# Optimization experiments

Measured on AMD Instinct MI355X. Metric: run time of the kernel, lower is better.

The kernel has to match this reference:

```python
import jax, jax.numpy as jnp
import numpy as np

N = 100000   # nodes
E = 1600000  # edges
IN = 128     # input feature dim
HID = 64     # hidden = IN // 2
OUT = 8      # output_size
B = 16384    # lookup batch


def sage_conv(x, src, dst, W_l, W_r, b, n):
    # PyG SAGEConv (aggr='mean', root_weight=True):
    # out = lin_l(mean_{j in N(i)} x_j) + lin_r(x_i)
    msgs = x[src]                                              # [E, F] gather
    agg = jax.ops.segment_sum(msgs, dst, num_segments=n)       # [N, F] scatter-add
    deg = jax.ops.segment_sum(jnp.ones((src.shape[0],), x.dtype), dst, num_segments=n)
    mean = agg / jnp.maximum(deg, 1.0)[:, None]                # zero-degree -> 0
    return mean @ W_l + x @ W_r + b


def setup_inputs() -> dict:
    key = jax.random.key(0)
    ks = jax.random.split(key, 10)
    node_feats = jax.random.normal(ks[0], (N, IN), dtype=jnp.float32)
    edge_index = jax.random.randint(ks[1], (2, E), 0, N, dtype=jnp.int64)
    idx = jax.random.randint(ks[2], (B,), 0, N, dtype=jnp.int64)
    dropout_mask = jax.random.uniform(ks[3], (N, HID), dtype=jnp.float32)
    s1 = 1.0 / np.sqrt(IN)
    s2 = 1.0 / np.sqrt(HID)
    W1_l = jax.random.normal(ks[4], (IN, HID), dtype=jnp.float32) * s1
    W1_r = jax.random.normal(ks[5], (IN, HID), dtype=jnp.float32) * s1
    b1 = jnp.zeros((HID,), dtype=jnp.float32)
    W2_l = jax.random.normal(ks[6], (HID, OUT), dtype=jnp.float32) * s2
    W2_r = jax.random.normal(ks[7], (HID, OUT), dtype=jnp.float32) * s2
    b2 = jnp.zeros((OUT,), dtype=jnp.float32)
    return {"node_feats": node_feats, "edge_index": edge_index, "idx": idx,
            "dropout_mask": dropout_mask, "W1_l": W1_l, "W1_r": W1_r, "b1": b1,
            "W2_l": W2_l, "W2_r": W2_r, "b2": b2}


def reference(node_feats, edge_index, idx, dropout_mask, W1_l, W1_r, b1, W2_l, W2_r, b2):
    n = node_feats.shape[0]
    src, dst = edge_index[0], edge_index[1]
    h = sage_conv(node_feats, src, dst, W1_l, W1_r, b1, n)     # [N, HID]
    h = jax.nn.relu(h)
    keep = (dropout_mask > 0.5).astype(h.dtype)                # F.dropout p=0.5
    h = h * keep * 2.0                                         # inverted dropout scale 1/(1-p)
    emb = sage_conv(h, src, dst, W2_l, W2_r, b2, n)            # [N, OUT]
    return emb[idx]                                            # [B, OUT]
```

## Files before the change

### kernel.cpp

```cpp
#include <hip/hip_runtime.h>
#include <hip/hip_fp16.h>

#define IN_F 128
#define HID_F 64
#define OUT_F 8

#define BSHIFT 7
#define BGRAN 128
#define BCAP 2688
#define NBUK_MAX 784
#define CHUNK 4096
#define EPT (CHUNK / 256)
#define CEPT ((BCAP + 255) / 256)

typedef _Float16 f16x8 __attribute__((ext_vector_type(8)));
typedef float f32x4 __attribute__((ext_vector_type(4)));

__global__ __launch_bounds__(1024) void init_bcur(int* __restrict__ bcur, int nbuk) {
  int t = threadIdx.x;
  if (t < nbuk) bcur[t] = t * BCAP;
}

__global__ __launch_bounds__(256) void mask_pack(
    const float* __restrict__ mask,
    unsigned long long* __restrict__ mbits, int n_nodes) {
  int wid = (blockIdx.x * 256 + threadIdx.x) >> 6;
  int lane = threadIdx.x & 63;
  int nw = (gridDim.x * 256) >> 6;
  int step = nw * 4;
  int node = wid * 4;
  for (; node + 4 <= n_nodes; node += step) {
    float m0 = mask[(size_t)(node + 0) * HID_F + lane];
    float m1 = mask[(size_t)(node + 1) * HID_F + lane];
    float m2 = mask[(size_t)(node + 2) * HID_F + lane];
    float m3 = mask[(size_t)(node + 3) * HID_F + lane];
    unsigned long long b0 = __ballot(m0 > 0.5f);
    unsigned long long b1 = __ballot(m1 > 0.5f);
    unsigned long long b2 = __ballot(m2 > 0.5f);
    unsigned long long b3 = __ballot(m3 > 0.5f);
    if (lane == 0) {
      mbits[node + 0] = b0;
      mbits[node + 1] = b1;
      mbits[node + 2] = b2;
      mbits[node + 3] = b3;
    }
  }
  if (node < n_nodes) {
    int rem = n_nodes - node;
    for (int u = 0; u < rem; ++u) {
      float mv = mask[(size_t)(node + u) * HID_F + lane];
      unsigned long long bb = __ballot(mv > 0.5f);
      if (lane == 0) mbits[node + u] = bb;
    }
  }
}

__global__ __launch_bounds__(256) void bucket_scatter(
    const int* __restrict__ src, const int* __restrict__ dst,
    int* __restrict__ bcur, int* __restrict__ ebuf, int n_edges) {
  __shared__ int hist[NBUK_MAX];
  __shared__ int base[NBUK_MAX];
  int t = threadIdx.x;
  for (int i = t; i < NBUK_MAX; i += 256) hist[i] = 0;
  __syncthreads();
  int e0 = blockIdx.x * CHUNK;
  int pk[EPT];
  int bk[EPT];
#pragma unroll
  for (int k = 0; k < EPT; ++k) {
    int e = e0 + k * 256 + t;
    if (e < n_edges) {
      int s = src[e];
      int d = dst[e];
      bk[k] = d >> BSHIFT;
      pk[k] = ((d & (BGRAN - 1)) << 24) | s;
      atomicAdd(&hist[bk[k]], 1);
    } else {
      bk[k] = -1;
    }
  }
  __syncthreads();
  for (int i = t; i < NBUK_MAX; i += 256) {
    int c = hist[i];
    base[i] = c ? atomicAdd(&bcur[i], c) : 0;
  }
  __syncthreads();
  for (int i = t; i < NBUK_MAX; i += 256) hist[i] = 0;
  __syncthreads();
#pragma unroll
  for (int k = 0; k < EPT; ++k) {
    if (bk[k] >= 0) {
      int r = atomicAdd(&hist[bk[k]], 1);
      ebuf[base[bk[k]] + r] = pk[k];
    }
  }
}

__global__ __launch_bounds__(256) void bucket_csr(
    const int* __restrict__ ebuf, const int* __restrict__ bcur,
    uint2* __restrict__ nd, int* __restrict__ csr_src, int n_nodes) {
  __shared__ int hist[BGRAN];
  __shared__ int cur[BGRAN];
  __shared__ int excl_s[BGRAN];
  __shared__ int lds_src[BCAP];
  int b = blockIdx.x;
  int t = threadIdx.x;
  if (t < BGRAN) hist[t] = 0;
  __syncthreads();
  int beg = b * BCAP;
  int cnt = bcur[b] - beg;
  int pk[CEPT];
  int np = 0;
  for (int j = t; j < cnt; j += 256) {
    pk[np] = ebuf[beg + j];
    atomicAdd(&hist[(unsigned)pk[np] >> 24], 1);
    ++np;
  }
  __syncthreads();
  if (t < 64) {
    int h0 = hist[2 * t];
    int h1 = hist[2 * t + 1];
    int ps = h0 + h1;
#pragma unroll
    for (int dd = 1; dd < 64; dd <<= 1) {
      int u = __shfl_up(ps, dd);
      if (t >= dd) ps += u;
    }
    excl_s[2 * t] = ps - h1 - h0;
    excl_s[2 * t + 1] = ps - h1;
  }
  __syncthreads();
  if (t < BGRAN) {
    int excl = excl_s[t];
    cur[t] = excl;
    int node = b * BGRAN + t;
    if (node < n_nodes) nd[node] = make_uint2((unsigned)(beg + excl), (unsigned)hist[t]);
  }
  __syncthreads();
  for (int i = 0; i < np; ++i) {
    int dl = (unsigned)pk[i] >> 24;
    int p = atomicAdd(&cur[dl], 1);
    lds_src[p] = pk[i] & 0xFFFFFF;
  }
  __syncthreads();
  for (int j = t; j < cnt; j += 256) csr_src[beg + j] = lds_src[j];
}

__global__ __launch_bounds__(256) void w_prep(
    const float* __restrict__ Wl, const float* __restrict__ Wr,
    _Float16* __restrict__ Wt) {
  int i = blockIdx.x * 256 + threadIdx.x;
  int n = i & 127;
  int k4 = (i >> 7) * 4;
  _Float16 hv[4];
#pragma unroll
  for (int j = 0; j < 4; ++j) {
    float v = (n < HID_F) ? Wl[(k4 + j) * HID_F + n]
                          : Wr[(k4 + j) * HID_F + (n - HID_F)];
    hv[j] = (_Float16)v;
  }
  *(uint2*)(Wt + (size_t)n * IN_F + k4) = *(uint2*)hv;
}

#define K1_ROWS 64
#define XSH 136
__global__ __launch_bounds__(256) void k1_proj(
    const float* __restrict__ x,
    const _Float16* __restrict__ Wt,
    const float* __restrict__ b1,
    __half* __restrict__ y1h,
    __half* __restrict__ r1h,
    int n_nodes) {
  __shared__ _Float16 XS[K1_ROWS * XSH];
  int tid = threadIdx.x;
  int w = tid >> 6;
  int lane = tid & 63;
  int n0 = blockIdx.x * K1_ROWS;
  int m = lane & 15;
  int quad = lane >> 4;

  f16x8 af[2][4];
#pragma unroll
  for (int ti = 0; ti < 2; ++ti) {
    int t = w + ti * 4;
#pragma unroll
    for (int kk = 0; kk < 4; ++kk)
      af[ti][kk] = *(const f16x8*)(Wt + (size_t)(t * 16 + m) * IN_F + kk * 32 + quad * 8);
  }
  float4 b1v = *(const float4*)(b1 + w * 16 + quad * 4);

#pragma unroll
  for (int p = 0; p < 8; ++p) {
    int i = tid + p * 256;
    int row = i >> 5;
    int k4 = (i & 31) * 4;
    int gs = min(n0 + row, n_nodes - 1);
    float4 v = *(const float4*)(x + (size_t)gs * IN_F + k4);
    _Float16 hv[4] = {(_Float16)v.x, (_Float16)v.y, (_Float16)v.z, (_Float16)v.w};
    *(uint2*)&XS[row * XSH + k4] = *(uint2*)hv;
  }
  __syncthreads();

#pragma unroll
  for (int rt = 0; rt < 4; ++rt) {
    f32x4 acc0 = f32x4{0.f, 0.f, 0.f, 0.f};
    f32x4 acc1 = f32x4{0.f, 0.f, 0.f, 0.f};
#pragma unroll
    for (int kk = 0; kk < 4; ++kk) {
      f16x8 bx = *(const f16x8*)&XS[(rt * 16 + m) * XSH + kk * 32 + quad * 8];
      acc0 = __builtin_amdgcn_mfma_f32_16x16x32_f16(af[0][kk], bx, acc0, 0, 0, 0);
      acc1 = __builtin_amdgcn_mfma_f32_16x16x32_f16(af[1][kk], bx, acc1, 0, 0, 0);
    }
    int node = n0 + rt * 16 + m;
    if (node < n_nodes) {
      __half hy[4], hr[4];
#pragma unroll
      for (int r = 0; r < 4; ++r) {
        hy[r] = __float2half(acc0[r]);
        hr[r] = __float2half(acc1[r] + ((const float*)&b1v)[r]);
      }
      *(uint2*)(y1h + (size_t)node * HID_F + w * 16 + quad * 4) = *(uint2*)hy;
      *(uint2*)(r1h + (size_t)node * HID_F + w * 16 + quad * 4) = *(uint2*)hr;
    }
  }
}

__global__ __launch_bounds__(256) void agg1_fused(
    const __half* __restrict__ y1h,
    const __half* __restrict__ r1h,
    const uint2* __restrict__ nd,
    const int* __restrict__ csr_src,
    const unsigned long long* __restrict__ mbits,
    __half* __restrict__ h_h,
    int n_nodes) {
  int node = (blockIdx.x * blockDim.x + threadIdx.x) >> 6;
  int lane = threadIdx.x & 63;
  if (node >= n_nodes) return;
  int nu = __builtin_amdgcn_readfirstlane(node);
  int q = lane >> 4;
  int f4 = lane & 15;

  uint2 be = nd[nu];
  unsigned long long mb = mbits[nu];
  size_t o = (size_t)nu * HID_F + f4 * 4;
  uint2 rg = *(const uint2*)(r1h + o);

  int beg = (int)be.x;
  int d = (int)be.y;
  const int* cp = csr_src + beg;
  float a0 = 0.f, a1 = 0.f, a2 = 0.f, a3 = 0.f;

#define ACC4(g)                                              \
  {                                                          \
    float2 p0 = __half22float2(*(const __half2*)&(g).x);     \
    float2 p1 = __half22float2(*(const __half2*)&(g).y);     \
    a0 += p0.x; a1 += p0.y; a2 += p1.x; a3 += p1.y;          \
  }

  int j = 0;
  for (; j + 32 <= d; j += 32) {
    int s0 = cp[j + q];
    int s1 = cp[j + 4 + q];
    int s2 = cp[j + 8 + q];
    int s3 = cp[j + 12 + q];
    int s4 = cp[j + 16 + q];
    int s5 = cp[j + 20 + q];
    int s6 = cp[j + 24 + q];
    int s7 = cp[j + 28 + q];
    uint2 g0 = *(const uint2*)(y1h + (size_t)s0 * HID_F + f4 * 4);
    uint2 g1 = *(const uint2*)(y1h + (size_t)s1 * HID_F + f4 * 4);
    uint2 g2 = *(const uint2*)(y1h + (size_t)s2 * HID_F + f4 * 4);
    uint2 g3 = *(const uint2*)(y1h + (size_t)s3 * HID_F + f4 * 4);
    uint2 g4 = *(const uint2*)(y1h + (size_t)s4 * HID_F + f4 * 4);
    uint2 g5 = *(const uint2*)(y1h + (size_t)s5 * HID_F + f4 * 4);
    uint2 g6 = *(const uint2*)(y1h + (size_t)s6 * HID_F + f4 * 4);
    uint2 g7 = *(const uint2*)(y1h + (size_t)s7 * HID_F + f4 * 4);
    ACC4(g0) ACC4(g1) ACC4(g2) ACC4(g3)
    ACC4(g4) ACC4(g5) ACC4(g6) ACC4(g7)
  }
  if (j + 16 <= d) {
    int s0 = cp[j + q];
    int s1 = cp[j + 4 + q];
    int s2 = cp[j + 8 + q];
    int s3 = cp[j + 12 + q];
    uint2 g0 = *(const uint2*)(y1h + (size_t)s0 * HID_F + f4 * 4);
    uint2 g1 = *(const uint2*)(y1h + (size_t)s1 * HID_F + f4 * 4);
    uint2 g2 = *(const uint2*)(y1h + (size_t)s2 * HID_F + f4 * 4);
    uint2 g3 = *(const uint2*)(y1h + (size_t)s3 * HID_F + f4 * 4);
    ACC4(g0) ACC4(g1) ACC4(g2) ACC4(g3)
    j += 16;
  }
  if (j < d) {
    int dm = d - 1;
    int e0 = j + q, e1 = j + 4 + q, e2 = j + 8 + q, e3 = j + 12 + q;
    int s0 = cp[min(e0, dm)];
    int s1 = cp[min(e1, dm)];
    int s2 = cp[min(e2, dm)];
    int s3 = cp[min(e3, dm)];
    uint2 g0 = *(const uint2*)(y1h + (size_t)s0 * HID_F + f4 * 4);
    uint2 g1 = *(const uint2*)(y1h + (size_t)s1 * HID_F + f4 * 4);
    uint2 g2 = *(const uint2*)(y1h + (size_t)s2 * HID_F + f4 * 4);
    uint2 g3 = *(const uint2*)(y1h + (size_t)s3 * HID_F + f4 * 4);
    if (e0 < d) ACC4(g0)
    if (e1 < d) ACC4(g1)
    if (e2 < d) ACC4(g2)
    if (e3 < d) ACC4(g3)
  }
#undef ACC4

  a0 += __shfl_xor(a0, 16); a0 += __shfl_xor(a0, 32);
  a1 += __shfl_xor(a1, 16); a1 += __shfl_xor(a1, 32);
  a2 += __shfl_xor(a2, 16); a2 += __shfl_xor(a2, 32);
  a3 += __shfl_xor(a3, 16); a3 += __shfl_xor(a3, 32);
  if (q == 0) {
    float inv = 1.0f / fmaxf((float)d, 1.0f);
    float2 r01 = __half22float2(*(const __half2*)&rg.x);
    float2 r23 = __half22float2(*(const __half2*)&rg.y);
    float vx = fmaxf(a0 * inv + r01.x, 0.f);
    float vy = fmaxf(a1 * inv + r01.y, 0.f);
    float vz = fmaxf(a2 * inv + r23.x, 0.f);
    float vw = fmaxf(a3 * inv + r23.y, 0.f);
    int fb = f4 * 4;
    vx = ((mb >> (fb + 0)) & 1ull) ? vx * 2.f : 0.f;
    vy = ((mb >> (fb + 1)) & 1ull) ? vy * 2.f : 0.f;
    vz = ((mb >> (fb + 2)) & 1ull) ? vz * 2.f : 0.f;
    vw = ((mb >> (fb + 3)) & 1ull) ? vw * 2.f : 0.f;
    __half hh[4] = {__float2half(vx), __float2half(vy),
                    __float2half(vz), __float2half(vw)};
    *(uint2*)(h_h + o) = *(uint2*)hh;
  }
}

__global__ __launch_bounds__(256) void k3b_z(
    const __half* __restrict__ h_h,
    const float* __restrict__ W2l,
    __half* __restrict__ z,
    int n_nodes) {
  __shared__ float WS[HID_F][OUT_F];
  int tid = threadIdx.x;
  if (tid < 128) {
    float4 w = *(const float4*)(W2l + tid * 4);
    *(float4*)&WS[tid >> 1][(tid & 1) * 4] = w;
  }
  __syncthreads();
  int node = blockIdx.x * blockDim.x + tid;
  if (node >= n_nodes) return;
  const __half* hr = h_h + (size_t)node * HID_F;
  float acc[8] = {0, 0, 0, 0, 0, 0, 0, 0};
  for (int k = 0; k < HID_F; k += 8) {
    uint4 hv = *(const uint4*)(hr + k);
    float2 f0 = __half22float2(*(const __half2*)&hv.x);
    float2 f1 = __half22float2(*(const __half2*)&hv.y);
    float2 f2 = __half22float2(*(const __half2*)&hv.z);
    float2 f3 = __half22float2(*(const __half2*)&hv.w);
    float hh[8] = {f0.x, f0.y, f1.x, f1.y, f2.x, f2.y, f3.x, f3.y};
#pragma unroll
    for (int j = 0; j < 8; ++j) {
      float4 w0 = *(const float4*)&WS[k + j][0];
      float4 w1 = *(const float4*)&WS[k + j][4];
      acc[0] += hh[j] * w0.x; acc[1] += hh[j] * w0.y;
      acc[2] += hh[j] * w0.z; acc[3] += hh[j] * w0.w;
      acc[4] += hh[j] * w1.x; acc[5] += hh[j] * w1.y;
      acc[6] += hh[j] * w1.z; acc[7] += hh[j] * w1.w;
    }
  }
  __half hz[8];
#pragma unroll
  for (int j = 0; j < 8; ++j) hz[j] = __float2half(acc[j]);
  *(uint4*)(z + (size_t)node * OUT_F) = *(uint4*)hz;
}

__global__ __launch_bounds__(256) void out_fused(
    const int* __restrict__ idx,
    const __half* __restrict__ z,
    const uint2* __restrict__ nd,
    const int* __restrict__ csr_src,
    const __half* __restrict__ h_h,
    const float* __restrict__ W2r,
    const float* __restrict__ b2,
    float* __restrict__ out,
    int n_batch) {
  int b = (blockIdx.x * blockDim.x + threadIdx.x) >> 6;
  int lane = threadIdx.x & 63;
  if (b >= n_batch) return;
  int bu = __builtin_amdgcn_readfirstlane(b);
  int i = idx[bu];
  int iu = __builtin_amdgcn_readfirstlane(i);
  int e8 = lane >> 3;
  int o = lane & 7;
  uint2 be = nd[iu];
  uint4 hv = *(const uint4*)(h_h + (size_t)iu * HID_F + e8 * 8);
  int beg = (int)be.x;
  int d = (int)be.y;
  const int* cp = csr_src + beg;
  float acc = 0.f;
  int j = e8;
  for (; j + 8 < d; j += 16) {
    int s0 = cp[j];
    int s1 = cp[j + 8];
    float z0 = __half2float(z[(size_t)s0 * OUT_F + o]);
    float z1 = __half2float(z[(size_t)s1 * OUT_F + o]);
    acc += z0 + z1;
  }
  if (j < d) acc += __half2float(z[(size_t)cp[j] * OUT_F + o]);
  float dv = fmaxf((float)d, 1.0f);
  float v = acc / dv;
  float2 f0 = __half22float2(*(const __half2*)&hv.x);
  float2 f1 = __half22float2(*(const __half2*)&hv.y);
  float2 f2 = __half22float2(*(const __half2*)&hv.z);
  float2 f3 = __half22float2(*(const __half2*)&hv.w);
  float hh[8] = {f0.x, f0.y, f1.x, f1.y, f2.x, f2.y, f3.x, f3.y};
#pragma unroll
  for (int jj = 0; jj < 8; ++jj) {
    int k = e8 * 8 + jj;
    v += hh[jj] * W2r[k * OUT_F + o];
  }
  v += __shfl_xor(v, 8);
  v += __shfl_xor(v, 16);
  v += __shfl_xor(v, 32);
  if (e8 == 0) out[(size_t)b * OUT_F + o] = v + b2[o];
}

extern "C" void kernel_launch(void* const* d_in, const int* in_sizes, int n_in,
                              void* d_out, int out_size, void* d_ws, size_t ws_size,
                              hipStream_t stream) {
  const float* x    = (const float*)d_in[0];
  const int*   ei   = (const int*)d_in[1];
  const int*   idx  = (const int*)d_in[2];
  const float* mask = (const float*)d_in[3];
  const float* W1l  = (const float*)d_in[4];
  const float* W1r  = (const float*)d_in[5];
  const float* b1   = (const float*)d_in[6];
  const float* W2l  = (const float*)d_in[7];
  const float* W2r  = (const float*)d_in[8];
  const float* b2   = (const float*)d_in[9];
  float* out = (float*)d_out;

  int n_nodes = in_sizes[0] / IN_F;
  int n_edges = in_sizes[1] / 2;
  int n_batch = in_sizes[2];
  const int* src = ei;
  const int* dst = ei + n_edges;

  int nbuk = (n_nodes + BGRAN - 1) / BGRAN;
  int nchunk = (n_edges + CHUNK - 1) / CHUNK;

  char* ws = (char*)d_ws;
  size_t off = 0;
  __half* y1h = (__half*)(ws + off); off += (size_t)n_nodes * HID_F * 2;
  __half* r1h = (__half*)(ws + off); off += (size_t)n_nodes * HID_F * 2;
  __half* h_h = (__half*)(ws + off); off += (size_t)n_nodes * HID_F * 2;
  __half* z   = (__half*)(ws + off); off += (size_t)n_nodes * OUT_F * 2;
  unsigned long long* mbits = (unsigned long long*)(ws + off); off += (size_t)n_nodes * 8;
  _Float16* Wt = (_Float16*)(ws + off); off += (size_t)IN_F * IN_F * 2;
  int* ebuf    = (int*)(ws + off); off += (size_t)nbuk * BCAP * 4;
  int* csr_src = (int*)(ws + off); off += (size_t)nbuk * BCAP * 4;
  uint2* nd    = (uint2*)(ws + off); off += (size_t)n_nodes * 8;
  int* bcur    = (int*)(ws + off); off += NBUK_MAX * 4;

  init_bcur<<<1, 1024, 0, stream>>>(bcur, nbuk);
  w_prep<<<16, 256, 0, stream>>>(W1l, W1r, Wt);
  mask_pack<<<1024, 256, 0, stream>>>(mask, mbits, n_nodes);
  bucket_scatter<<<nchunk, 256, 0, stream>>>(src, dst, bcur, ebuf, n_edges);
  k1_proj<<<(n_nodes + K1_ROWS - 1) / K1_ROWS, 256, 0, stream>>>(
      x, Wt, b1, y1h, r1h, n_nodes);
  bucket_csr<<<nbuk, 256, 0, stream>>>(ebuf, bcur, nd, csr_src, n_nodes);

  {
    long long th = (long long)n_nodes * HID_F;
    agg1_fused<<<(int)((th + 255) / 256), 256, 0, stream>>>(
        y1h, r1h, nd, csr_src, mbits, h_h, n_nodes);
  }

  k3b_z<<<(n_nodes + 255) / 256, 256, 0, stream>>>(h_h, W2l, z, n_nodes);
  {
    long long th = (long long)n_batch * 64;
    out_fused<<<(int)((th + 255) / 256), 256, 0, stream>>>(
        idx, z, nd, csr_src, h_h, W2r, b2, out, n_batch);
  }
}
```

Measured before the change: 225.8 us.

## Merge prep kernels, drop mask packing, use fp16 partial sums and 32-bit gather offsets

Merges init_bcur and w_prep into a single prep launch and removes the mask_pack kernel. agg1 now reads the float dropout mask row directly instead of packed bits. The agg1 gather loop drops from 32 to 16 edges per iteration and sums four neighbours in half2 before converting to float. Gather addresses in agg1 and out_fused use unsigned 32-bit shifts instead of size_t multiplies. This removes two launches and a full mask pass, but half-precision partial sums reduce accuracy and the shorter loop gives less memory-level parallelism.

```diff
diff --git a/kernel.cpp b/kernel.cpp
--- a/kernel.cpp
+++ b/kernel.cpp
@@ -16,42 +16,24 @@
 typedef _Float16 f16x8 __attribute__((ext_vector_type(8)));
 typedef float f32x4 __attribute__((ext_vector_type(4)));
 
-__global__ __launch_bounds__(1024) void init_bcur(int* __restrict__ bcur, int nbuk) {
-  int t = threadIdx.x;
-  if (t < nbuk) bcur[t] = t * BCAP;
-}
-
-__global__ __launch_bounds__(256) void mask_pack(
-    const float* __restrict__ mask,
-    unsigned long long* __restrict__ mbits, int n_nodes) {
-  int wid = (blockIdx.x * 256 + threadIdx.x) >> 6;
-  int lane = threadIdx.x & 63;
-  int nw = (gridDim.x * 256) >> 6;
-  int step = nw * 4;
-  int node = wid * 4;
-  for (; node + 4 <= n_nodes; node += step) {
-    float m0 = mask[(size_t)(node + 0) * HID_F + lane];
-    float m1 = mask[(size_t)(node + 1) * HID_F + lane];
-    float m2 = mask[(size_t)(node + 2) * HID_F + lane];
-    float m3 = mask[(size_t)(node + 3) * HID_F + lane];
-    unsigned long long b0 = __ballot(m0 > 0.5f);
-    unsigned long long b1 = __ballot(m1 > 0.5f);
-    unsigned long long b2 = __ballot(m2 > 0.5f);
-    unsigned long long b3 = __ballot(m3 > 0.5f);
-    if (lane == 0) {
-      mbits[node + 0] = b0;
-      mbits[node + 1] = b1;
-      mbits[node + 2] = b2;
-      mbits[node + 3] = b3;
-    }
-  }
-  if (node < n_nodes) {
-    int rem = n_nodes - node;
-    for (int u = 0; u < rem; ++u) {
-      float mv = mask[(size_t)(node + u) * HID_F + lane];
-      unsigned long long bb = __ballot(mv > 0.5f);
-      if (lane == 0) mbits[node + u] = bb;
-    }
+__global__ __launch_bounds__(256) void prep(
+    const float* __restrict__ Wl, const float* __restrict__ Wr,
+    _Float16* __restrict__ Wt, int* __restrict__ bcur, int nbuk) {
+  int blk = blockIdx.x;
+  if (blk < 16) {
+    int i = blk * 256 + threadIdx.x;
+    int n = i & 127;
+    int k4 = (i >> 7) * 4;
+    _Float16 hv[4];
+#pragma unroll
+    for (int j = 0; j < 4; ++j) {
+      float v = (n < HID_F) ? Wl[(k4 + j) * HID_F + n]
+                            : Wr[(k4 + j) * HID_F + (n - HID_F)];
+      hv[j] = (_Float16)v;
+    }
+    *(uint2*)(Wt + (size_t)n * IN_F + k4) = *(uint2*)hv;
+  } else {
+    for (int i = threadIdx.x; i < nbuk; i += 256) bcur[i] = i * BCAP;
   }
 }
 
@@ -144,22 +126,6 @@
   }
   __syncthreads();
   for (int j = t; j < cnt; j += 256) csr_src[beg + j] = lds_src[j];
-}
-
-__global__ __launch_bounds__(256) void w_prep(
-    const float* __restrict__ Wl, const float* __restrict__ Wr,
-    _Float16* __restrict__ Wt) {
-  int i = blockIdx.x * 256 + threadIdx.x;
-  int n = i & 127;
-  int k4 = (i >> 7) * 4;
-  _Float16 hv[4];
-#pragma unroll
-  for (int j = 0; j < 4; ++j) {
-    float v = (n < HID_F) ? Wl[(k4 + j) * HID_F + n]
-                          : Wr[(k4 + j) * HID_F + (n - HID_F)];
-    hv[j] = (_Float16)v;
-  }
-  *(uint2*)(Wt + (size_t)n * IN_F + k4) = *(uint2*)hv;
 }
 
 #define K1_ROWS 64
@@ -230,7 +196,7 @@
     const __half* __restrict__ r1h,
     const uint2* __restrict__ nd,
     const int* __restrict__ csr_src,
-    const unsigned long long* __restrict__ mbits,
+    const float* __restrict__ mask,
     __half* __restrict__ h_h,
     int n_nodes) {
   int node = (blockIdx.x * blockDim.x + threadIdx.x) >> 6;
@@ -241,72 +207,67 @@
   int f4 = lane & 15;
 
   uint2 be = nd[nu];
-  unsigned long long mb = mbits[nu];
   size_t o = (size_t)nu * HID_F + f4 * 4;
   uint2 rg = *(const uint2*)(r1h + o);
+  float4 mrow = *(const float4*)(mask + (size_t)nu * HID_F + f4 * 4);
 
   int beg = (int)be.x;
   int d = (int)be.y;
   const int* cp = csr_src + beg;
+  const char* yb = (const char*)y1h;
+  unsigned foff = (unsigned)(f4 * 8);
+
   float a0 = 0.f, a1 = 0.f, a2 = 0.f, a3 = 0.f;
-
-#define ACC4(g)                                              \
-  {                                                          \
-    float2 p0 = __half22float2(*(const __half2*)&(g).x);     \
-    float2 p1 = __half22float2(*(const __half2*)&(g).y);     \
-    a0 += p0.x; a1 += p0.y; a2 += p1.x; a3 += p1.y;          \
-  }
-
   int j = 0;
-  for (; j + 32 <= d; j += 32) {
-    int s0 = cp[j + q];
-    int s1 = cp[j + 4 + q];
-    int s2 = cp[j + 8 + q];
-    int s3 = cp[j + 12 + q];
-    int s4 = cp[j + 16 + q];
-    int s5 = cp[j + 20 + q];
-    int s6 = cp[j + 24 + q];
-    int s7 = cp[j + 28 + q];
-    uint2 g0 = *(const uint2*)(y1h + (size_t)s0 * HID_F + f4 * 4);
-    uint2 g1 = *(const uint2*)(y1h + (size_t)s1 * HID_F + f4 * 4);
-    uint2 g2 = *(const uint2*)(y1h + (size_t)s2 * HID_F + f4 * 4);
-    uint2 g3 = *(const uint2*)(y1h + (size_t)s3 * HID_F + f4 * 4);
-    uint2 g4 = *(const uint2*)(y1h + (size_t)s4 * HID_F + f4 * 4);
-    uint2 g5 = *(const uint2*)(y1h + (size_t)s5 * HID_F + f4 * 4);
-    uint2 g6 = *(const uint2*)(y1h + (size_t)s6 * HID_F + f4 * 4);
-    uint2 g7 = *(const uint2*)(y1h + (size_t)s7 * HID_F + f4 * 4);
-    ACC4(g0) ACC4(g1) ACC4(g2) ACC4(g3)
-    ACC4(g4) ACC4(g5) ACC4(g6) ACC4(g7)
-  }
-  if (j + 16 <= d) {
-    int s0 = cp[j + q];
-    int s1 = cp[j + 4 + q];
-    int s2 = cp[j + 8 + q];
-    int s3 = cp[j + 12 + q];
-    uint2 g0 = *(const uint2*)(y1h + (size_t)s0 * HID_F + f4 * 4);
-    uint2 g1 = *(const uint2*)(y1h + (size_t)s1 * HID_F + f4 * 4);
-    uint2 g2 = *(const uint2*)(y1h + (size_t)s2 * HID_F + f4 * 4);
-    uint2 g3 = *(const uint2*)(y1h + (size_t)s3 * HID_F + f4 * 4);
-    ACC4(g0) ACC4(g1) ACC4(g2) ACC4(g3)
-    j += 16;
+  for (; j + 16 <= d; j += 16) {
+    unsigned s0 = (unsigned)cp[j + q];
+    unsigned s1 = (unsigned)cp[j + 4 + q];
+    unsigned s2 = (unsigned)cp[j + 8 + q];
+    unsigned s3 = (unsigned)cp[j + 12 + q];
+    uint2 g0 = *(const uint2*)(yb + ((s0 << 7) + foff));
+    uint2 g1 = *(const uint2*)(yb + ((s1 << 7) + foff));
+    uint2 g2 = *(const uint2*)(yb + ((s2 << 7) + foff));
+    uint2 g3 = *(const uint2*)(yb + ((s3 << 7) + foff));
+    __half2 hx = *(const __half2*)&g0.x;
+    __half2 hy = *(const __half2*)&g0.y;
+    hx = __hadd2(hx, *(const __half2*)&g1.x);
+    hy = __hadd2(hy, *(const __half2*)&g1.y);
+    hx = __hadd2(hx, *(const __half2*)&g2.x);
+    hy = __hadd2(hy, *(const __half2*)&g2.y);
+    hx = __hadd2(hx, *(const __half2*)&g3.x);
+    hy = __hadd2(hy, *(const __half2*)&g3.y);
+    float2 fx = __half22float2(hx);
+    float2 fy = __half22float2(hy);
+    a0 += fx.x; a1 += fx.y; a2 += fy.x; a3 += fy.y;
   }
   if (j < d) {
     int dm = d - 1;
     int e0 = j + q, e1 = j + 4 + q, e2 = j + 8 + q, e3 = j + 12 + q;
-    int s0 = cp[min(e0, dm)];
-    int s1 = cp[min(e1, dm)];
-    int s2 = cp[min(e2, dm)];
-    int s3 = cp[min(e3, dm)];
-    uint2 g0 = *(const uint2*)(y1h + (size_t)s0 * HID_F + f4 * 4);
-    uint2 g1 = *(const uint2*)(y1h + (size_t)s1 * HID_F + f4 * 4);
-    uint2 g2 = *(const uint2*)(y1h + (size_t)s2 * HID_F + f4 * 4);
-    uint2 g3 = *(const uint2*)(y1h + (size_t)s3 * HID_F + f4 * 4);
-    if (e0 < d) ACC4(g0)
-    if (e1 < d) ACC4(g1)
-    if (e2 < d) ACC4(g2)
-    if (e3 < d) ACC4(g3)
-  }
-#undef ACC4
+    unsigned s0 = (unsigned)cp[min(e0, dm)];
+    unsigned s1 = (unsigned)cp[min(e1, dm)];
+    unsigned s2 = (unsigned)cp[min(e2, dm)];
+    unsigned s3 = (unsigned)cp[min(e3, dm)];
+    uint2 g0 = *(const uint2*)(yb + ((s0 << 7) + foff));
+    uint2 g1 = *(const uint2*)(yb + ((s1 << 7) + foff));
+    uint2 g2 = *(const uint2*)(yb + ((s2 << 7) + foff));
+    uint2 g3 = *(const uint2*)(yb + ((s3 << 7) + foff));
+    uint2 zz = make_uint2(0u, 0u);
+    if (e0 >= d) g0 = zz;
+    if (e1 >= d) g1 = zz;
+    if (e2 >= d) g2 = zz;
+    if (e3 >= d) g3 = zz;
+    __half2 hx = *(const __half2*)&g0.x;
+    __half2 hy = *(const __half2*)&g0.y;
+    hx = __hadd2(hx, *(const __half2*)&g1.x);
+    hy = __hadd2(hy, *(const __half2*)&g1.y);
+    hx = __hadd2(hx, *(const __half2*)&g2.x);
+    hy = __hadd2(hy, *(const __half2*)&g2.y);
+    hx = __hadd2(hx, *(const __half2*)&g3.x);
+    hy = __hadd2(hy, *(const __half2*)&g3.y);
+    float2 fx = __half22float2(hx);
+    float2 fy = __half22float2(hy);
+    a0 += fx.x; a1 += fx.y; a2 += fy.x; a3 += fy.y;
+  }
 
   a0 += __shfl_xor(a0, 16); a0 += __shfl_xor(a0, 32);
   a1 += __shfl_xor(a1, 16); a1 += __shfl_xor(a1, 32);
@@ -320,11 +281,10 @@
     float vy = fmaxf(a1 * inv + r01.y, 0.f);
     float vz = fmaxf(a2 * inv + r23.x, 0.f);
     float vw = fmaxf(a3 * inv + r23.y, 0.f);
-    int fb = f4 * 4;
-    vx = ((mb >> (fb + 0)) & 1ull) ? vx * 2.f : 0.f;
-    vy = ((mb >> (fb + 1)) & 1ull) ? vy * 2.f : 0.f;
-    vz = ((mb >> (fb + 2)) & 1ull) ? vz * 2.f : 0.f;
-    vw = ((mb >> (fb + 3)) & 1ull) ? vw * 2.f : 0.f;
+    vx = (mrow.x > 0.5f) ? vx * 2.f : 0.f;
+    vy = (mrow.y > 0.5f) ? vy * 2.f : 0.f;
+    vz = (mrow.z > 0.5f) ? vz * 2.f : 0.f;
+    vw = (mrow.w > 0.5f) ? vw * 2.f : 0.f;
     __half hh[4] = {__float2half(vx), __float2half(vy),
                     __float2half(vz), __float2half(vw)};
     *(uint2*)(h_h + o) = *(uint2*)hh;
@@ -393,16 +353,21 @@
   int beg = (int)be.x;
   int d = (int)be.y;
   const int* cp = csr_src + beg;
+  const char* zb = (const char*)z;
+  unsigned ooff = (unsigned)(o * 2);
   float acc = 0.f;
   int j = e8;
   for (; j + 8 < d; j += 16) {
-    int s0 = cp[j];
-    int s1 = cp[j + 8];
-    float z0 = __half2float(z[(size_t)s0 * OUT_F + o]);
-    float z1 = __half2float(z[(size_t)s1 * OUT_F + o]);
+    unsigned s0 = (unsigned)cp[j];
+    unsigned s1 = (unsigned)cp[j + 8];
+    float z0 = __half2float(*(const __half*)(zb + ((s0 << 4) + ooff)));
+    float z1 = __half2float(*(const __half*)(zb + ((s1 << 4) + ooff)));
     acc += z0 + z1;
   }
-  if (j < d) acc += __half2float(z[(size_t)cp[j] * OUT_F + o]);
+  if (j < d) {
+    unsigned s0 = (unsigned)cp[j];
+    acc += __half2float(*(const __half*)(zb + ((s0 << 4) + ooff)));
+  }
   float dv = fmaxf((float)d, 1.0f);
   float v = acc / dv;
   float2 f0 = __half22float2(*(const __half2*)&hv.x);
@@ -451,16 +416,13 @@
   __half* r1h = (__half*)(ws + off); off += (size_t)n_nodes * HID_F * 2;
   __half* h_h = (__half*)(ws + off); off += (size_t)n_nodes * HID_F * 2;
   __half* z   = (__half*)(ws + off); off += (size_t)n_nodes * OUT_F * 2;
-  unsigned long long* mbits = (unsigned long long*)(ws + off); off += (size_t)n_nodes * 8;
   _Float16* Wt = (_Float16*)(ws + off); off += (size_t)IN_F * IN_F * 2;
   int* ebuf    = (int*)(ws + off); off += (size_t)nbuk * BCAP * 4;
   int* csr_src = (int*)(ws + off); off += (size_t)nbuk * BCAP * 4;
   uint2* nd    = (uint2*)(ws + off); off += (size_t)n_nodes * 8;
   int* bcur    = (int*)(ws + off); off += NBUK_MAX * 4;
 
-  init_bcur<<<1, 1024, 0, stream>>>(bcur, nbuk);
-  w_prep<<<16, 256, 0, stream>>>(W1l, W1r, Wt);
-  mask_pack<<<1024, 256, 0, stream>>>(mask, mbits, n_nodes);
+  prep<<<17, 256, 0, stream>>>(W1l, W1r, Wt, bcur, nbuk);
   bucket_scatter<<<nchunk, 256, 0, stream>>>(src, dst, bcur, ebuf, n_edges);
   k1_proj<<<(n_nodes + K1_ROWS - 1) / K1_ROWS, 256, 0, stream>>>(
       x, Wt, b1, y1h, r1h, n_nodes);
@@ -469,7 +431,7 @@
   {
     long long th = (long long)n_nodes * HID_F;
     agg1_fused<<<(int)((th + 255) / 256), 256, 0, stream>>>(
-        y1h, r1h, nd, csr_src, mbits, h_h, n_nodes);
+        y1h, r1h, nd, csr_src, mask, h_h, n_nodes);
   }
 
   k3b_z<<<(n_nodes + 255) / 256, 256, 0, stream>>>(h_h, W2l, z, n_nodes);
```

New measurement: 224.5 us. Within noise of the previous version (-0.6%).
